# Optimization experiments

Hardware: AMD Instinct MI355X
Metric: run time of the kernel (lower is better)

## Reference

```python
import jax, jax.numpy as jnp
import numpy as np

B, T, ND, SD, H = 4096, 256, 16, 8, 64
IN = SD + ND  # LSTM input dim


def setup_inputs() -> dict:
    key = jax.random.key(0)
    ks = jax.random.split(key, 20)
    def w(k, shape):
        fan_in = shape[0]
        return jax.random.normal(k, shape, jnp.float32) / np.sqrt(fan_in)
    return {
        "noise": jax.random.normal(ks[0], (B, T - 1, ND), jnp.float32),
        "eps": jax.random.normal(ks[1], (B, T - 1, SD), jnp.float32),
        "Wx": w(ks[2], (IN, 4 * H)),
        "Wh": w(ks[3], (H, 4 * H)),
        "b": jnp.zeros((4 * H,), jnp.float32),
        "Wm1": w(ks[4], (H, H)), "bm1": jnp.zeros((H,), jnp.float32),
        "Wm2": w(ks[5], (H, H)), "bm2": jnp.zeros((H,), jnp.float32),
        "Wm3": w(ks[6], (H, SD)), "bm3": jnp.zeros((SD,), jnp.float32),
        "Wv1": w(ks[7], (H, H)), "bv1": jnp.zeros((H,), jnp.float32),
        "Wv2": w(ks[8], (H, H)), "bv2": jnp.zeros((H,), jnp.float32),
        "Wv3": w(ks[9], (H, SD)), "bv3": jnp.zeros((SD,), jnp.float32),
    }


def reference(noise, eps, Wx, Wh, b, Wm1, bm1, Wm2, bm2, Wm3, bm3,
              Wv1, bv1, Wv2, bv2, Wv3, bv3):
    Bn = noise.shape[0]
    Hn = Wh.shape[0]
    Dn = Wm3.shape[1]

    def mlp(h, W1, b1, W2, b2, W3, b3):
        a = jax.nn.relu(h @ W1 + b1)
        a = jax.nn.relu(a @ W2 + b2)
        return a @ W3 + b3

    def step(carry, inp_t):
        x, h, c = carry
        n_t, e_t = inp_t
        # Keras LSTM: gates ordered i, f, g(cell), o
        z = jnp.concatenate([x, n_t], axis=-1) @ Wx + h @ Wh + b  # [B, 4H]
        i, f, g, o = jnp.split(z, 4, axis=-1)
        c = jax.nn.sigmoid(f) * c + jax.nn.sigmoid(i) * jnp.tanh(g)
        h = jax.nn.sigmoid(o) * jnp.tanh(c)
        mu = mlp(h, Wm1, bm1, Wm2, bm2, Wm3, bm3)
        std = jnp.exp(0.5 * mlp(h, Wv1, bv1, Wv2, bv2, Wv3, bv3))
        x = mu + std * e_t  # reparameterized Normal(mu, std).sample()
        return (x, h, c), x

    x0 = jnp.zeros((Bn, Dn), noise.dtype)  # log_series=True -> zeros
    h0 = jnp.zeros((Bn, Hn), noise.dtype)
    c0 = jnp.zeros((Bn, Hn), noise.dtype)
    noise_t = jnp.swapaxes(noise, 0, 1)  # [T-1, B, ND]
    eps_t = jnp.swapaxes(eps, 0, 1)      # [T-1, B, SD]
    _, xs = jax.lax.scan(step, (x0, h0, c0), (noise_t, eps_t))
    seq = jnp.concatenate([x0[:, None, :], jnp.swapaxes(xs, 0, 1)], axis=1)  # [B, T, SD]
    return jnp.cumsum(seq, axis=1)
```

## Files before the change

kernel.cpp:

```cpp
#include <hip/hip_runtime.h>

typedef _Float16 half8 __attribute__((ext_vector_type(8)));
typedef float f32x4 __attribute__((ext_vector_type(4)));

#define TSTEPS 255
#define R 16
#define BLK 512
#define XS 100
#define ZS 260
#define AS 68

__device__ __forceinline__ float frcp(float x) { return __builtin_amdgcn_rcpf(x); }

__device__ __forceinline__ f32x4 mfma16(half8 a, half8 b, f32x4 c) {
  return __builtin_amdgcn_mfma_f32_16x16x32_f16(a, b, c, 0, 0, 0);
}

__device__ __forceinline__ void ldcvt8(const float* p, half8& hi, half8& lo) {
  const float4 u = *(const float4*)p;
  const float4 v = *(const float4*)(p + 4);
  const float a[8] = {u.x, u.y, u.z, u.w, v.x, v.y, v.z, v.w};
  #pragma unroll
  for (int j = 0; j < 8; ++j) {
    _Float16 h = (_Float16)a[j];
    hi[j] = h;
    lo[j] = (_Float16)(a[j] - (float)h);
  }
}

__global__ __launch_bounds__(BLK)
void genlstm_kernel(const float* __restrict__ noise,
                    const float* __restrict__ eps,
                    const float* __restrict__ Wx,
                    const float* __restrict__ Wh,
                    const float* __restrict__ bg,
                    const float* __restrict__ Wm1, const float* __restrict__ bm1,
                    const float* __restrict__ Wm2, const float* __restrict__ bm2,
                    const float* __restrict__ Wm3, const float* __restrict__ bm3,
                    const float* __restrict__ Wv1, const float* __restrict__ bv1,
                    const float* __restrict__ Wv2, const float* __restrict__ bv2,
                    const float* __restrict__ Wv3, const float* __restrict__ bv3,
                    float* __restrict__ out)
{
  __shared__ __align__(16) float xin[R][XS];
  __shared__ __align__(16) float z2[R][ZS];
  __shared__ __align__(16) float a1[2][R][AS];
  __shared__ __align__(16) float a2[2][R][AS];
  __shared__ __align__(16) float mulv[2][R][9];

  const int tid  = threadIdx.x;
  const int w    = tid >> 6;
  const int l    = tid & 63;
  const int lrow = l & 15;
  const int lq   = l >> 4;
  const long rowbase = (long)blockIdx.x * R;

  half8 gBhi[2][3], gBlo[2][3];
  #pragma unroll
  for (int t = 0; t < 2; ++t)
    #pragma unroll
    for (int kt = 0; kt < 3; ++kt)
      #pragma unroll
      for (int j = 0; j < 8; ++j) {
        int k = 32 * kt + 8 * lq + j;
        int n = 32 * w + 16 * t + lrow;
        float v = 0.f;
        if (k < 24) v = Wx[k * 256 + n];
        else if (k < 88) v = Wh[(k - 24) * 256 + n];
        _Float16 h = (_Float16)v;
        gBhi[t][kt][j] = h;
        gBlo[t][kt][j] = (_Float16)(v - (float)h);
      }

  const int chain = w >> 2;
  const int nt = w & 3;
  const float* W1 = chain ? Wv1 : Wm1;
  const float* W2 = chain ? Wv2 : Wm2;
  half8 B1hi[2], B1lo[2], B2hi[2], B2lo[2];
  #pragma unroll
  for (int kt = 0; kt < 2; ++kt)
    #pragma unroll
    for (int j = 0; j < 8; ++j) {
      int k = 32 * kt + 8 * lq + j;
      int n = 16 * nt + lrow;
      float v1 = W1[k * 64 + n];
      _Float16 h1 = (_Float16)v1;
      B1hi[kt][j] = h1; B1lo[kt][j] = (_Float16)(v1 - (float)h1);
      float v2 = W2[k * 64 + n];
      _Float16 h2 = (_Float16)v2;
      B2hi[kt][j] = h2; B2lo[kt][j] = (_Float16)(v2 - (float)h2);
    }

  half8 B3hi[2], B3lo[2];
  if (w < 2) {
    const float* W3 = w ? Wv3 : Wm3;
    #pragma unroll
    for (int kt = 0; kt < 2; ++kt)
      #pragma unroll
      for (int j = 0; j < 8; ++j) {
        int k = 32 * kt + 8 * lq + j;
        float v = (lrow < 8) ? W3[k * 8 + lrow] : 0.f;
        _Float16 h = (_Float16)v;
        B3hi[kt][j] = h;
        B3lo[kt][j] = (_Float16)(v - (float)h);
      }
  }

  const float bias1 = (chain ? bv1 : bm1)[16 * nt + lrow];
  const float bias2 = (chain ? bv2 : bm2)[16 * nt + lrow];
  float bias3 = 0.f;
  if (w < 2 && lrow < 8) bias3 = (w ? bv3 : bm3)[lrow];

  const float bgi = bg[l], bgf = bg[64 + l], bgg = bg[128 + l], bgo = bg[192 + l];

  float cst0 = 0.f, cst1 = 0.f;
  const int r5 = tid >> 3, d5 = tid & 7;
  float cum = 0.f;

  for (int i = tid; i < R * XS; i += BLK) (&xin[0][0])[i] = 0.f;
  if (tid < 128) out[((rowbase + r5) * 256) * 8 + d5] = 0.f;
  __syncthreads();

  float4 nz = {0.f, 0.f, 0.f, 0.f};
  if (tid < 64) {
    int r = tid >> 2, j4 = (tid & 3) * 4;
    *(float4*)&xin[r][8 + j4] =
        *(const float4*)&noise[((rowbase + r) * TSTEPS) * 16 + j4];
    nz = *(const float4*)&noise[((rowbase + r) * TSTEPS + 1) * 16 + j4];
  }
  float ev = 0.f;
  if (tid < 128) ev = eps[((rowbase + r5) * TSTEPS) * 8 + d5];
  __syncthreads();

  for (int ts = 0; ts < TSTEPS; ++ts) {
    half8 Ahi[3], Alo[3];
    #pragma unroll
    for (int kt = 0; kt < 3; ++kt)
      ldcvt8(&xin[lrow][32 * kt + 8 * lq], Ahi[kt], Alo[kt]);

    f32x4 accz0 = {0.f, 0.f, 0.f, 0.f};
    f32x4 accz1 = {0.f, 0.f, 0.f, 0.f};
    #pragma unroll
    for (int kt = 0; kt < 3; ++kt) {
      accz0 = mfma16(Ahi[kt], gBhi[0][kt], accz0);
      accz1 = mfma16(Ahi[kt], gBhi[1][kt], accz1);
      accz0 = mfma16(Alo[kt], gBhi[0][kt], accz0);
      accz1 = mfma16(Alo[kt], gBhi[1][kt], accz1);
      accz0 = mfma16(Ahi[kt], gBlo[0][kt], accz0);
      accz1 = mfma16(Ahi[kt], gBlo[1][kt], accz1);
    }
    {
      const int r0 = 4 * lq;
      #pragma unroll
      for (int k = 0; k < 4; ++k) {
        z2[r0 + k][32 * w + lrow]      = accz0[k];
        z2[r0 + k][32 * w + 16 + lrow] = accz1[k];
      }
    }
    __syncthreads();

    #pragma unroll
    for (int rr = 0; rr < 2; ++rr) {
      const int r = w + rr * 8;
      float zi = z2[r][l]       + bgi;
      float zf = z2[r][64 + l]  + bgf;
      float zg = z2[r][128 + l] + bgg;
      float zo = z2[r][192 + l] + bgo;
      float si = frcp(1.f + __expf(-zi));
      float sf = frcp(1.f + __expf(-zf));
      float so = frcp(1.f + __expf(-zo));
      float ag = fabsf(zg), eg = __expf(-2.f * ag);
      float tg = copysignf((1.f - eg) * frcp(1.f + eg), zg);
      float cs = rr ? cst1 : cst0;
      cs = fmaf(sf, cs, si * tg);
      if (rr) cst1 = cs; else cst0 = cs;
      float ac = fabsf(cs), ec = __expf(-2.f * ac);
      float tc = copysignf((1.f - ec) * frcp(1.f + ec), cs);
      xin[r][24 + l] = so * tc;
    }
    if (tid < 64) {
      int r = tid >> 2, j4 = (tid & 3) * 4;
      *(float4*)&xin[r][8 + j4] = nz;
      if (ts + 2 < TSTEPS)
        nz = *(const float4*)&noise[((rowbase + r) * TSTEPS + ts + 2) * 16 + j4];
    }
    __syncthreads();

    {
      half8 hhi[2], hlo[2];
      #pragma unroll
      for (int kt = 0; kt < 2; ++kt)
        ldcvt8(&xin[lrow][24 + 32 * kt + 8 * lq], hhi[kt], hlo[kt]);
      f32x4 acc = {0.f, 0.f, 0.f, 0.f};
      #pragma unroll
      for (int kt = 0; kt < 2; ++kt) {
        acc = mfma16(hhi[kt], B1hi[kt], acc);
        acc = mfma16(hlo[kt], B1hi[kt], acc);
        acc = mfma16(hhi[kt], B1lo[kt], acc);
      }
      const int r0 = 4 * lq;
      #pragma unroll
      for (int k = 0; k < 4; ++k)
        a1[chain][r0 + k][16 * nt + lrow] = fmaxf(acc[k] + bias1, 0.f);
    }
    __syncthreads();

    {
      half8 ahi[2], alo[2];
      #pragma unroll
      for (int kt = 0; kt < 2; ++kt)
        ldcvt8(&a1[chain][lrow][32 * kt + 8 * lq], ahi[kt], alo[kt]);
      f32x4 acc = {0.f, 0.f, 0.f, 0.f};
      #pragma unroll
      for (int kt = 0; kt < 2; ++kt) {
        acc = mfma16(ahi[kt], B2hi[kt], acc);
        acc = mfma16(alo[kt], B2hi[kt], acc);
        acc = mfma16(ahi[kt], B2lo[kt], acc);
      }
      const int r0 = 4 * lq;
      #pragma unroll
      for (int k = 0; k < 4; ++k)
        a2[chain][r0 + k][16 * nt + lrow] = fmaxf(acc[k] + bias2, 0.f);
    }
    __syncthreads();

    if (w < 2) {
      half8 chi[2], clo[2];
      #pragma unroll
      for (int kt = 0; kt < 2; ++kt)
        ldcvt8(&a2[w][lrow][32 * kt + 8 * lq], chi[kt], clo[kt]);
      f32x4 acc = {0.f, 0.f, 0.f, 0.f};
      #pragma unroll
      for (int kt = 0; kt < 2; ++kt) {
        acc = mfma16(chi[kt], B3hi[kt], acc);
        acc = mfma16(clo[kt], B3hi[kt], acc);
        acc = mfma16(chi[kt], B3lo[kt], acc);
      }
      if (lrow < 8) {
        const int r0 = 4 * lq;
        #pragma unroll
        for (int k = 0; k < 4; ++k)
          mulv[w][r0 + k][lrow] = acc[k] + bias3;
      }
    }
    __syncthreads();

    if (tid < 128) {
      float mu = mulv[0][r5][d5];
      float lv = mulv[1][r5][d5];
      float x = fmaf(__expf(0.5f * lv), ev, mu);
      cum += x;
      out[((rowbase + r5) * 256 + ts + 1) * 8 + d5] = cum;
      xin[r5][d5] = x;
      if (ts + 1 < TSTEPS)
        ev = eps[((rowbase + r5) * TSTEPS + ts + 1) * 8 + d5];
    }
    __syncthreads();
  }
}

extern "C" void kernel_launch(void* const* d_in, const int* in_sizes, int n_in,
                              void* d_out, int out_size, void* d_ws, size_t ws_size,
                              hipStream_t stream) {
  const float* noise = (const float*)d_in[0];
  const float* eps   = (const float*)d_in[1];
  const float* Wx    = (const float*)d_in[2];
  const float* Wh    = (const float*)d_in[3];
  const float* bg    = (const float*)d_in[4];
  const float* Wm1   = (const float*)d_in[5];
  const float* bm1   = (const float*)d_in[6];
  const float* Wm2   = (const float*)d_in[7];
  const float* bm2   = (const float*)d_in[8];
  const float* Wm3   = (const float*)d_in[9];
  const float* bm3   = (const float*)d_in[10];
  const float* Wv1   = (const float*)d_in[11];
  const float* bv1   = (const float*)d_in[12];
  const float* Wv2   = (const float*)d_in[13];
  const float* bv2   = (const float*)d_in[14];
  const float* Wv3   = (const float*)d_in[15];
  const float* bv3   = (const float*)d_in[16];
  float* out = (float*)d_out;

  dim3 grid(4096 / R), block(BLK);
  hipLaunchKernelGGL(genlstm_kernel, grid, block, 0, stream,
                     noise, eps, Wx, Wh, bg, Wm1, bm1, Wm2, bm2, Wm3, bm3,
                     Wv1, bv1, Wv2, bv2, Wv3, bv3, out);
}
```

Measured before the change: 663.7 us.

## Store activations as split fp16 hi/lo in LDS and interleave gate columns

Activations in shared memory (x, h, MLP hidden layers) are now split into fp16 hi/lo pairs once, by the producing thread, instead of being stored as fp32 and re-split by every consumer before each MFMA. The input vector is reordered so h comes first, and h fragments are kept in registers from the previous step's MLP load for the gate matmul. Gate weight columns are permuted so each lane's i/f/g/o values are contiguous and read with one float4 load. This cuts LDS traffic and conversion ALU work on the serial per-step critical path. The cost is extra shared arrays and a more involved index mapping.

```diff
diff --git a/kernel.cpp b/kernel.cpp
--- a/kernel.cpp
+++ b/kernel.cpp
@@ -1,31 +1,20 @@
 #include <hip/hip_runtime.h>
 
 typedef _Float16 half8 __attribute__((ext_vector_type(8)));
+typedef _Float16 half4 __attribute__((ext_vector_type(4)));
 typedef float f32x4 __attribute__((ext_vector_type(4)));
 
 #define TSTEPS 255
 #define R 16
 #define BLK 512
-#define XS 100
+#define XSH 104
 #define ZS 260
-#define AS 68
+#define ASH 72
 
 __device__ __forceinline__ float frcp(float x) { return __builtin_amdgcn_rcpf(x); }
 
 __device__ __forceinline__ f32x4 mfma16(half8 a, half8 b, f32x4 c) {
   return __builtin_amdgcn_mfma_f32_16x16x32_f16(a, b, c, 0, 0, 0);
-}
-
-__device__ __forceinline__ void ldcvt8(const float* p, half8& hi, half8& lo) {
-  const float4 u = *(const float4*)p;
-  const float4 v = *(const float4*)(p + 4);
-  const float a[8] = {u.x, u.y, u.z, u.w, v.x, v.y, v.z, v.w};
-  #pragma unroll
-  for (int j = 0; j < 8; ++j) {
-    _Float16 h = (_Float16)a[j];
-    hi[j] = h;
-    lo[j] = (_Float16)(a[j] - (float)h);
-  }
 }
 
 __global__ __launch_bounds__(BLK)
@@ -42,11 +31,14 @@
                     const float* __restrict__ Wv3, const float* __restrict__ bv3,
                     float* __restrict__ out)
 {
-  __shared__ __align__(16) float xin[R][XS];
-  __shared__ __align__(16) float z2[R][ZS];
-  __shared__ __align__(16) float a1[2][R][AS];
-  __shared__ __align__(16) float a2[2][R][AS];
-  __shared__ __align__(16) float mulv[2][R][9];
+  __shared__ __align__(16) _Float16 xh[R][XSH];
+  __shared__ __align__(16) _Float16 xl[R][XSH];
+  __shared__ __align__(16) float    z2[R][ZS];
+  __shared__ __align__(16) _Float16 a1h[2][R][ASH];
+  __shared__ __align__(16) _Float16 a1l[2][R][ASH];
+  __shared__ __align__(16) _Float16 a2h[2][R][ASH];
+  __shared__ __align__(16) _Float16 a2l[2][R][ASH];
+  __shared__ __align__(16) float    mulv[2][R][12];
 
   const int tid  = threadIdx.x;
   const int w    = tid >> 6;
@@ -62,11 +54,12 @@
     for (int kt = 0; kt < 3; ++kt)
       #pragma unroll
       for (int j = 0; j < 8; ++j) {
-        int k = 32 * kt + 8 * lq + j;
-        int n = 32 * w + 16 * t + lrow;
+        int k  = 32 * kt + 8 * lq + j;
+        int jc = 32 * w + 16 * t + lrow;
+        int n  = 64 * (jc & 3) + (jc >> 2);
         float v = 0.f;
-        if (k < 24) v = Wx[k * 256 + n];
-        else if (k < 88) v = Wh[(k - 24) * 256 + n];
+        if (k < 64) v = Wh[k * 256 + n];
+        else if (k < 88) v = Wx[(k - 64) * 256 + n];
         _Float16 h = (_Float16)v;
         gBhi[t][kt][j] = h;
         gBlo[t][kt][j] = (_Float16)(v - (float)h);
@@ -111,21 +104,38 @@
   float bias3 = 0.f;
   if (w < 2 && lrow < 8) bias3 = (w ? bv3 : bm3)[lrow];
 
-  const float bgi = bg[l], bgf = bg[64 + l], bgg = bg[128 + l], bgo = bg[192 + l];
+  const float4 bgq = {bg[l], bg[64 + l], bg[128 + l], bg[192 + l]};
 
   float cst0 = 0.f, cst1 = 0.f;
   const int r5 = tid >> 3, d5 = tid & 7;
   float cum = 0.f;
 
-  for (int i = tid; i < R * XS; i += BLK) (&xin[0][0])[i] = 0.f;
+  half8 hHi[2], hLo[2];
+  #pragma unroll
+  for (int kt = 0; kt < 2; ++kt)
+    #pragma unroll
+    for (int j = 0; j < 8; ++j) { hHi[kt][j] = (_Float16)0; hLo[kt][j] = (_Float16)0; }
+
+  for (int i = tid; i < R * XSH; i += BLK) {
+    (&xh[0][0])[i] = (_Float16)0;
+    (&xl[0][0])[i] = (_Float16)0;
+  }
   if (tid < 128) out[((rowbase + r5) * 256) * 8 + d5] = 0.f;
   __syncthreads();
 
   float4 nz = {0.f, 0.f, 0.f, 0.f};
   if (tid < 64) {
     int r = tid >> 2, j4 = (tid & 3) * 4;
-    *(float4*)&xin[r][8 + j4] =
-        *(const float4*)&noise[((rowbase + r) * TSTEPS) * 16 + j4];
+    float4 n0 = *(const float4*)&noise[((rowbase + r) * TSTEPS) * 16 + j4];
+    float tmp[4] = {n0.x, n0.y, n0.z, n0.w};
+    half4 nh, nl;
+    #pragma unroll
+    for (int j = 0; j < 4; ++j) {
+      _Float16 h = (_Float16)tmp[j];
+      nh[j] = h; nl[j] = (_Float16)(tmp[j] - (float)h);
+    }
+    *(half4*)&xh[r][72 + j4] = nh;
+    *(half4*)&xl[r][72 + j4] = nl;
     nz = *(const float4*)&noise[((rowbase + r) * TSTEPS + 1) * 16 + j4];
   }
   float ev = 0.f;
@@ -133,22 +143,29 @@
   __syncthreads();
 
   for (int ts = 0; ts < TSTEPS; ++ts) {
-    half8 Ahi[3], Alo[3];
-    #pragma unroll
-    for (int kt = 0; kt < 3; ++kt)
-      ldcvt8(&xin[lrow][32 * kt + 8 * lq], Ahi[kt], Alo[kt]);
+    half8 Xhi = *(const half8*)&xh[lrow][64 + 8 * lq];
+    half8 Xlo = *(const half8*)&xl[lrow][64 + 8 * lq];
 
     f32x4 accz0 = {0.f, 0.f, 0.f, 0.f};
     f32x4 accz1 = {0.f, 0.f, 0.f, 0.f};
-    #pragma unroll
-    for (int kt = 0; kt < 3; ++kt) {
-      accz0 = mfma16(Ahi[kt], gBhi[0][kt], accz0);
-      accz1 = mfma16(Ahi[kt], gBhi[1][kt], accz1);
-      accz0 = mfma16(Alo[kt], gBhi[0][kt], accz0);
-      accz1 = mfma16(Alo[kt], gBhi[1][kt], accz1);
-      accz0 = mfma16(Ahi[kt], gBlo[0][kt], accz0);
-      accz1 = mfma16(Ahi[kt], gBlo[1][kt], accz1);
-    }
+    accz0 = mfma16(hHi[0], gBhi[0][0], accz0);
+    accz1 = mfma16(hHi[0], gBhi[1][0], accz1);
+    accz0 = mfma16(hLo[0], gBhi[0][0], accz0);
+    accz1 = mfma16(hLo[0], gBhi[1][0], accz1);
+    accz0 = mfma16(hHi[0], gBlo[0][0], accz0);
+    accz1 = mfma16(hHi[0], gBlo[1][0], accz1);
+    accz0 = mfma16(hHi[1], gBhi[0][1], accz0);
+    accz1 = mfma16(hHi[1], gBhi[1][1], accz1);
+    accz0 = mfma16(hLo[1], gBhi[0][1], accz0);
+    accz1 = mfma16(hLo[1], gBhi[1][1], accz1);
+    accz0 = mfma16(hHi[1], gBlo[0][1], accz0);
+    accz1 = mfma16(hHi[1], gBlo[1][1], accz1);
+    accz0 = mfma16(Xhi, gBhi[0][2], accz0);
+    accz1 = mfma16(Xhi, gBhi[1][2], accz1);
+    accz0 = mfma16(Xlo, gBhi[0][2], accz0);
+    accz1 = mfma16(Xlo, gBhi[1][2], accz1);
+    accz0 = mfma16(Xhi, gBlo[0][2], accz0);
+    accz1 = mfma16(Xhi, gBlo[1][2], accz1);
     {
       const int r0 = 4 * lq;
       #pragma unroll
@@ -162,10 +179,11 @@
     #pragma unroll
     for (int rr = 0; rr < 2; ++rr) {
       const int r = w + rr * 8;
-      float zi = z2[r][l]       + bgi;
-      float zf = z2[r][64 + l]  + bgf;
-      float zg = z2[r][128 + l] + bgg;
-      float zo = z2[r][192 + l] + bgo;
+      float4 zq = *(const float4*)&z2[r][4 * l];
+      float zi = zq.x + bgq.x;
+      float zf = zq.y + bgq.y;
+      float zg = zq.z + bgq.z;
+      float zo = zq.w + bgq.w;
       float si = frcp(1.f + __expf(-zi));
       float sf = frcp(1.f + __expf(-zf));
       float so = frcp(1.f + __expf(-zo));
@@ -176,66 +194,85 @@
       if (rr) cst1 = cs; else cst0 = cs;
       float ac = fabsf(cs), ec = __expf(-2.f * ac);
       float tc = copysignf((1.f - ec) * frcp(1.f + ec), cs);
-      xin[r][24 + l] = so * tc;
+      float hv = so * tc;
+      _Float16 hh = (_Float16)hv;
+      xh[r][l] = hh;
+      xl[r][l] = (_Float16)(hv - (float)hh);
     }
     if (tid < 64) {
       int r = tid >> 2, j4 = (tid & 3) * 4;
-      *(float4*)&xin[r][8 + j4] = nz;
+      float tmp[4] = {nz.x, nz.y, nz.z, nz.w};
+      half4 nh, nl;
+      #pragma unroll
+      for (int j = 0; j < 4; ++j) {
+        _Float16 h = (_Float16)tmp[j];
+        nh[j] = h; nl[j] = (_Float16)(tmp[j] - (float)h);
+      }
+      *(half4*)&xh[r][72 + j4] = nh;
+      *(half4*)&xl[r][72 + j4] = nl;
       if (ts + 2 < TSTEPS)
         nz = *(const float4*)&noise[((rowbase + r) * TSTEPS + ts + 2) * 16 + j4];
     }
     __syncthreads();
 
     {
-      half8 hhi[2], hlo[2];
-      #pragma unroll
-      for (int kt = 0; kt < 2; ++kt)
-        ldcvt8(&xin[lrow][24 + 32 * kt + 8 * lq], hhi[kt], hlo[kt]);
+      hHi[0] = *(const half8*)&xh[lrow][8 * lq];
+      hHi[1] = *(const half8*)&xh[lrow][32 + 8 * lq];
+      hLo[0] = *(const half8*)&xl[lrow][8 * lq];
+      hLo[1] = *(const half8*)&xl[lrow][32 + 8 * lq];
       f32x4 acc = {0.f, 0.f, 0.f, 0.f};
       #pragma unroll
       for (int kt = 0; kt < 2; ++kt) {
-        acc = mfma16(hhi[kt], B1hi[kt], acc);
-        acc = mfma16(hlo[kt], B1hi[kt], acc);
-        acc = mfma16(hhi[kt], B1lo[kt], acc);
+        acc = mfma16(hHi[kt], B1hi[kt], acc);
+        acc = mfma16(hLo[kt], B1hi[kt], acc);
+        acc = mfma16(hHi[kt], B1lo[kt], acc);
       }
       const int r0 = 4 * lq;
       #pragma unroll
-      for (int k = 0; k < 4; ++k)
-        a1[chain][r0 + k][16 * nt + lrow] = fmaxf(acc[k] + bias1, 0.f);
+      for (int k = 0; k < 4; ++k) {
+        float v = fmaxf(acc[k] + bias1, 0.f);
+        _Float16 vh = (_Float16)v;
+        a1h[chain][r0 + k][16 * nt + lrow] = vh;
+        a1l[chain][r0 + k][16 * nt + lrow] = (_Float16)(v - (float)vh);
+      }
     }
     __syncthreads();
 
     {
-      half8 ahi[2], alo[2];
-      #pragma unroll
-      for (int kt = 0; kt < 2; ++kt)
-        ldcvt8(&a1[chain][lrow][32 * kt + 8 * lq], ahi[kt], alo[kt]);
+      half8 ahi0 = *(const half8*)&a1h[chain][lrow][8 * lq];
+      half8 ahi1 = *(const half8*)&a1h[chain][lrow][32 + 8 * lq];
+      half8 alo0 = *(const half8*)&a1l[chain][lrow][8 * lq];
+      half8 alo1 = *(const half8*)&a1l[chain][lrow][32 + 8 * lq];
       f32x4 acc = {0.f, 0.f, 0.f, 0.f};
-      #pragma unroll
-      for (int kt = 0; kt < 2; ++kt) {
-        acc = mfma16(ahi[kt], B2hi[kt], acc);
-        acc = mfma16(alo[kt], B2hi[kt], acc);
-        acc = mfma16(ahi[kt], B2lo[kt], acc);
-      }
+      acc = mfma16(ahi0, B2hi[0], acc);
+      acc = mfma16(alo0, B2hi[0], acc);
+      acc = mfma16(ahi0, B2lo[0], acc);
+      acc = mfma16(ahi1, B2hi[1], acc);
+      acc = mfma16(alo1, B2hi[1], acc);
+      acc = mfma16(ahi1, B2lo[1], acc);
       const int r0 = 4 * lq;
       #pragma unroll
-      for (int k = 0; k < 4; ++k)
-        a2[chain][r0 + k][16 * nt + lrow] = fmaxf(acc[k] + bias2, 0.f);
+      for (int k = 0; k < 4; ++k) {
+        float v = fmaxf(acc[k] + bias2, 0.f);
+        _Float16 vh = (_Float16)v;
+        a2h[chain][r0 + k][16 * nt + lrow] = vh;
+        a2l[chain][r0 + k][16 * nt + lrow] = (_Float16)(v - (float)vh);
+      }
     }
     __syncthreads();
 
     if (w < 2) {
-      half8 chi[2], clo[2];
-      #pragma unroll
-      for (int kt = 0; kt < 2; ++kt)
-        ldcvt8(&a2[w][lrow][32 * kt + 8 * lq], chi[kt], clo[kt]);
+      half8 chi0 = *(const half8*)&a2h[w][lrow][8 * lq];
+      half8 chi1 = *(const half8*)&a2h[w][lrow][32 + 8 * lq];
+      half8 clo0 = *(const half8*)&a2l[w][lrow][8 * lq];
+      half8 clo1 = *(const half8*)&a2l[w][lrow][32 + 8 * lq];
       f32x4 acc = {0.f, 0.f, 0.f, 0.f};
-      #pragma unroll
-      for (int kt = 0; kt < 2; ++kt) {
-        acc = mfma16(chi[kt], B3hi[kt], acc);
-        acc = mfma16(clo[kt], B3hi[kt], acc);
-        acc = mfma16(chi[kt], B3lo[kt], acc);
-      }
+      acc = mfma16(chi0, B3hi[0], acc);
+      acc = mfma16(clo0, B3hi[0], acc);
+      acc = mfma16(chi0, B3lo[0], acc);
+      acc = mfma16(chi1, B3hi[1], acc);
+      acc = mfma16(clo1, B3hi[1], acc);
+      acc = mfma16(chi1, B3lo[1], acc);
       if (lrow < 8) {
         const int r0 = 4 * lq;
         #pragma unroll
@@ -251,7 +288,9 @@
       float x = fmaf(__expf(0.5f * lv), ev, mu);
       cum += x;
       out[((rowbase + r5) * 256 + ts + 1) * 8 + d5] = cum;
-      xin[r5][d5] = x;
+      _Float16 xhh = (_Float16)x;
+      xh[r5][64 + d5] = xhh;
+      xl[r5][64 + d5] = (_Float16)(x - (float)xhh);
       if (ts + 1 < TSTEPS)
         ev = eps[((rowbase + r5) * TSTEPS + ts + 1) * 8 + d5];
     }
```

After: 589.1 us. 1.13x faster.
